# Performance work log

Measured on AMD Instinct MI355X. Metric: run time of the kernel, lower is better.

Reference implementation:

```python
import jax, jax.numpy as jnp
import numpy as np

Ts = 1.0  # simulation time step from netParams['simulation']


def _alpha_filter(x, tau):
    # Causal SRM-alpha PSP filter along time (leading axis):
    #   y[t] = Ts * sum_{k>=0} (k*Ts/tau) * exp(1 - k*Ts/tau) * x[t-k]
    # Implemented as an exact 2-state linear recurrence (IIR form of the alpha kernel).
    d = jnp.float32(np.exp(-Ts / tau))
    c = jnp.float32(np.e * Ts / tau * Ts)  # kernel scale * Ts integration factor

    def step(carry, xt):
        P, Q = carry           # P[t] = sum x[j] d^{t-j}; Q[t] = sum x[j] (t-j) d^{t-j}
        Q = d * (Q + P)
        P = d * P + xt
        return (P, Q), c * Q

    z = jnp.zeros_like(x[0])
    _, y = jax.lax.scan(step, (z, z), x)
    return y


def _make_spike(theta, tauRho, scaleRho):
    # SLAYER spike function: Heaviside forward, surrogate-gradient backward
    pdf_scale = scaleRho / (tauRho * theta)
    pdf_tc = tauRho * theta

    @jax.custom_vjp
    def spike(u):
        return (u >= theta).astype(u.dtype)

    def fwd(u):
        return spike(u), u

    def bwd(u, g):
        return (g * pdf_scale * jnp.exp(-jnp.abs(u - theta) / pdf_tc),)

    spike.defvjp(fwd, bwd)
    return spike


def _lif_spike(u_in, theta, tauRef, scaleRef, tauRho, scaleRho):
    # Sequential leaky integrate-and-fire with alpha refractory kernel:
    #   u[t] = u_in[t] - scaleRef*theta * sum_{j<t} s[j] * (dt/tauRef)*exp(1-dt/tauRef), dt=(t-j)*Ts
    # Refractory alpha kernel realized by the same 2-state recurrence, fed by emitted spikes.
    d = jnp.float32(np.exp(-Ts / tauRef))
    ref_gain = jnp.float32(scaleRef * theta * np.e * Ts / tauRef)
    spike = _make_spike(theta, tauRho, scaleRho)

    def step(carry, ut):
        P, Q = carry
        Q = d * (Q + P)            # refractory kernel value (zero at lag 0)
        s = spike(ut - ref_gain * Q)
        P = d * P + s              # inject this step's spikes
        return (P, Q), s

    z = jnp.zeros_like(u_in[0])
    _, s = jax.lax.scan(step, (z, z), u_in)
    return s


def _conv2d_t(x, w, pad):
    # x: [T, N, C, H, W] -> same spatial conv applied at every timestep (slayer conv = Conv3d with kT=1)
    T, N, C, H, W = x.shape
    y = jax.lax.conv_general_dilated(
        x.reshape(T * N, C, H, W), w,
        window_strides=(1, 1), padding=[(pad, pad), (pad, pad)],
        dimension_numbers=('NCHW', 'OIHW', 'NCHW'))
    return y.reshape(T, N, -1, H, W)


def _forward(spikeInput, conv1_w, conv2_w):
    # spikeInput: [N, C, H, W, T] -> scan over leading time axis
    x = jnp.transpose(spikeInput, (4, 0, 1, 2, 3))
    psp1 = _alpha_filter(x, tau=1.0)                                        # slayer1.psp (tauSr=1)
    s1 = _lif_spike(_conv2d_t(psp1, conv1_w, 2),
                    theta=30.0, tauRef=1.0, scaleRef=1.0, tauRho=1.0, scaleRho=10.0)
    psp2 = _alpha_filter(s1, tau=2.0)                                       # slayer2.psp (tauSr=2)
    s2 = _lif_spike(_conv2d_t(psp2, conv2_w, 1),
                    theta=50.0, tauRef=2.0, scaleRef=1.0, tauRho=1.0, scaleRho=10.0)
    return jnp.transpose(s2, (1, 2, 3, 4, 0))  # back to [N, C, H, W, T]


def setup_inputs() -> dict:
    key = jax.random.key(0)
    k1, k2, k3 = jax.random.split(key, 3)
    spikeInput = (jax.random.uniform(k1, (2, 8, 128, 128, 64)) < 0.1).astype(jnp.float32)
    # slayer conv uses weightScale-amplified weights, bias-free; scale so thresholds are reachable
    conv1_w = jax.random.normal(k2, (8, 8, 5, 5), jnp.float32) * 2.0
    conv2_w = jax.random.normal(k3, (8, 8, 3, 3), jnp.float32) * 2.0
    return {"spikeInput": spikeInput, "conv1_w": conv1_w, "conv2_w": conv2_w}


def reference(spikeInput, conv1_w, conv2_w):
    return _forward(spikeInput, conv1_w, conv2_w)
```

## Files before the change

kernel.cpp:

```cpp
#include <hip/hip_runtime.h>

#define TN 64
#define NB 2
#define CH 8
#define HH 128
#define WW 128
#define HW (HH*WW)
#define CHW (CH*HW)
#define NCHW (NB*CHW)

__global__ __launch_bounds__(256) void k_psp1(const float* __restrict__ x,
                                              float* __restrict__ psp1) {
    int e = blockIdx.x * blockDim.x + threadIdx.x;
    if (e >= NCHW) return;
    const float d1 = 0.36787944117144233f;
    const float c1 = 2.7182818284590452f;
    float P = 0.f, Q = 0.f;
    const float4* xe = reinterpret_cast<const float4*>(x + (size_t)e * TN);
    #pragma unroll
    for (int t4 = 0; t4 < TN / 4; ++t4) {
        float4 xv = xe[t4];
        float xs[4] = {xv.x, xv.y, xv.z, xv.w};
        #pragma unroll
        for (int j = 0; j < 4; ++j) {
            Q = d1 * (Q + P);
            P = d1 * P + xs[j];
            psp1[(size_t)(t4 * 4 + j) * NCHW + e] = c1 * Q;
        }
    }
}

__global__ __launch_bounds__(256, 4) void k_conv1(const float* __restrict__ in,
                                                  const float* __restrict__ w1,
                                                  float* __restrict__ outp) {
    __shared__ __align__(16) float tile[2][12][136];
    const int img = blockIdx.y;
    const int h0 = blockIdx.x * 8;
    const int tid = threadIdx.x;
    const int lx = tid & 31;
    const int yi = tid >> 5;
    const int x0 = lx * 4;
    const float* base = in + (size_t)img * CHW;
    float* lds = &tile[0][0][0];

    float acc[CH][4];
    #pragma unroll
    for (int co = 0; co < CH; ++co)
        #pragma unroll
        for (int xo = 0; xo < 4; ++xo) acc[co][xo] = 0.f;

    for (int cig = 0; cig < 4; ++cig) {
        const int ci0 = cig * 2;
        if (cig) __syncthreads();
        for (int slot = tid; slot < 1632; slot += 256) {
            int r = slot / 136;
            int c = slot - r * 136;
            int gh = h0 + r - 2, gw = c - 2;
            bool ok = (gh >= 0 && gh < HH && gw >= 0 && gw < WW);
            int g = gh * WW + gw;
            lds[slot]        = ok ? base[ci0 * HW + g]       : 0.f;
            lds[1632 + slot] = ok ? base[(ci0 + 1) * HW + g] : 0.f;
        }
        __syncthreads();

        #pragma unroll
        for (int c = 0; c < 2; ++c) {
            const int ci = ci0 + c;
            const float* chp = lds + c * 1632;
            #pragma unroll
            for (int ky = 0; ky < 5; ++ky) {
                const float4* rp =
                    reinterpret_cast<const float4*>(chp + (yi + ky) * 136 + x0);
                float4 a = rp[0], b = rp[1];
                float f[8] = {a.x, a.y, a.z, a.w, b.x, b.y, b.z, b.w};
                #pragma unroll
                for (int co = 0; co < CH; ++co) {
                    const float* wp = w1 + (co * CH + ci) * 25 + ky * 5;
                    #pragma unroll
                    for (int kx = 0; kx < 5; ++kx) {
                        float wv = wp[kx];
                        #pragma unroll
                        for (int xo = 0; xo < 4; ++xo)
                            acc[co][xo] = fmaf(wv, f[kx + xo], acc[co][xo]);
                    }
                }
            }
        }
    }

    float* ob = outp + (size_t)img * CHW + (h0 + yi) * WW + x0;
    #pragma unroll
    for (int co = 0; co < CH; ++co)
        *reinterpret_cast<float4*>(ob + co * HW) =
            make_float4(acc[co][0], acc[co][1], acc[co][2], acc[co][3]);
}

__global__ __launch_bounds__(256) void k_lif1_psp2(const float* __restrict__ u1,
                                                   float* __restrict__ psp2) {
    int e = blockIdx.x * blockDim.x + threadIdx.x;
    if (e >= NCHW) return;
    const float dr = 0.36787944117144233f;
    const float rg = 81.54845485377136f;
    const float th = 30.f;
    const float d2 = 0.60653065971263342f;
    const float c2 = 1.35914091422952262f;
    float Pr = 0.f, Qr = 0.f, P2 = 0.f, Q2 = 0.f;
    #pragma unroll 8
    for (int t = 0; t < TN; ++t) {
        Qr = dr * (Qr + Pr);
        float u = u1[(size_t)t * NCHW + e];
        float s = (u - rg * Qr >= th) ? 1.0f : 0.0f;
        Pr = dr * Pr + s;
        Q2 = d2 * (Q2 + P2);
        P2 = d2 * P2 + s;
        psp2[(size_t)t * NCHW + e] = c2 * Q2;
    }
}

__global__ __launch_bounds__(256, 4) void k_conv2(const float* __restrict__ in,
                                                  const float* __restrict__ w2,
                                                  float* __restrict__ outp) {
    __shared__ __align__(16) float tile[2][10][136];
    const int img = blockIdx.y;
    const int h0 = blockIdx.x * 8;
    const int tid = threadIdx.x;
    const int lx = tid & 31;
    const int yi = tid >> 5;
    const int x0 = lx * 4;
    const float* base = in + (size_t)img * CHW;
    float* lds = &tile[0][0][0];

    float acc[CH][4];
    #pragma unroll
    for (int co = 0; co < CH; ++co)
        #pragma unroll
        for (int xo = 0; xo < 4; ++xo) acc[co][xo] = 0.f;

    for (int cig = 0; cig < 4; ++cig) {
        const int ci0 = cig * 2;
        if (cig) __syncthreads();
        for (int slot = tid; slot < 1360; slot += 256) {
            int r = slot / 136;
            int c = slot - r * 136;
            int gh = h0 + r - 1, gw = c - 1;
            bool ok = (gh >= 0 && gh < HH && gw >= 0 && gw < WW);
            int g = gh * WW + gw;
            lds[slot]        = ok ? base[ci0 * HW + g]       : 0.f;
            lds[1360 + slot] = ok ? base[(ci0 + 1) * HW + g] : 0.f;
        }
        __syncthreads();

        #pragma unroll
        for (int c = 0; c < 2; ++c) {
            const int ci = ci0 + c;
            const float* chp = lds + c * 1360;
            #pragma unroll
            for (int ky = 0; ky < 3; ++ky) {
                const float4* rp =
                    reinterpret_cast<const float4*>(chp + (yi + ky) * 136 + x0);
                float4 a = rp[0], b = rp[1];
                float f[8] = {a.x, a.y, a.z, a.w, b.x, b.y, b.z, b.w};
                #pragma unroll
                for (int co = 0; co < CH; ++co) {
                    const float* wp = w2 + (co * CH + ci) * 9 + ky * 3;
                    #pragma unroll
                    for (int kx = 0; kx < 3; ++kx) {
                        float wv = wp[kx];
                        #pragma unroll
                        for (int xo = 0; xo < 4; ++xo)
                            acc[co][xo] = fmaf(wv, f[kx + xo], acc[co][xo]);
                    }
                }
            }
        }
    }

    float* ob = outp + (size_t)img * CHW + (h0 + yi) * WW + x0;
    #pragma unroll
    for (int co = 0; co < CH; ++co)
        *reinterpret_cast<float4*>(ob + co * HW) =
            make_float4(acc[co][0], acc[co][1], acc[co][2], acc[co][3]);
}

__global__ __launch_bounds__(256) void k_lif2(const float* __restrict__ u2,
                                              float* __restrict__ outp) {
    int e = blockIdx.x * blockDim.x + threadIdx.x;
    if (e >= NCHW) return;
    const float dr = 0.60653065971263342f;
    const float rg = 67.95704571147613f;
    const float th = 50.f;
    float Pr = 0.f, Qr = 0.f;
    float sv[TN];
    #pragma unroll
    for (int t = 0; t < TN; ++t) {
        Qr = dr * (Qr + Pr);
        float u = u2[(size_t)t * NCHW + e];
        float s = (u - rg * Qr >= th) ? 1.0f : 0.0f;
        Pr = dr * Pr + s;
        sv[t] = s;
    }
    float4* o = reinterpret_cast<float4*>(outp + (size_t)e * TN);
    #pragma unroll
    for (int i = 0; i < TN / 4; ++i)
        o[i] = make_float4(sv[4 * i], sv[4 * i + 1], sv[4 * i + 2], sv[4 * i + 3]);
}

extern "C" void kernel_launch(void* const* d_in, const int* in_sizes, int n_in,
                              void* d_out, int out_size, void* d_ws, size_t ws_size,
                              hipStream_t stream) {
    const float* x  = (const float*)d_in[0];
    const float* w1 = (const float*)d_in[1];
    const float* w2 = (const float*)d_in[2];
    float* out = (float*)d_out;

    float* bufA = (float*)d_ws;
    float* bufB = bufA + (size_t)TN * NCHW;

    dim3 blk(256);
    dim3 grd_pt(NCHW / 256);
    dim3 grd_cv(16, TN * NB);

    k_psp1<<<grd_pt, blk, 0, stream>>>(x, bufA);
    k_conv1<<<grd_cv, blk, 0, stream>>>(bufA, w1, bufB);
    k_lif1_psp2<<<grd_pt, blk, 0, stream>>>(bufB, bufA);
    k_conv2<<<grd_cv, blk, 0, stream>>>(bufA, w2, bufB);
    k_lif2<<<grd_pt, blk, 0, stream>>>(bufB, out);
}
```

Baseline: 216.1 us.

## Double-buffer conv input tiles with register prefetch of next channel pair

Both conv kernels now double-buffer the shared-memory tile and prefetch the next channel pair's halo values from global memory into registers before the compute phase. Global offsets are precomputed once per thread instead of recomputed each channel group. This removes one barrier per iteration and is meant to overlap global load latency with the FMA loop. The cost is doubled LDS usage and extra registers (up to 14 floats plus 7 offsets), which may hurt occupancy under launch_bounds(256,4).

After: 204.7 us. -5.3%, faster.

```diff
diff --git a/kernel.cpp b/kernel.cpp
--- a/kernel.cpp
+++ b/kernel.cpp
@@ -33,15 +33,34 @@
 __global__ __launch_bounds__(256, 4) void k_conv1(const float* __restrict__ in,
                                                   const float* __restrict__ w1,
                                                   float* __restrict__ outp) {
-    __shared__ __align__(16) float tile[2][12][136];
+    __shared__ __align__(16) float tile[2][2][12][136];
     const int img = blockIdx.y;
     const int h0 = blockIdx.x * 8;
     const int tid = threadIdx.x;
-    const int lx = tid & 31;
     const int yi = tid >> 5;
-    const int x0 = lx * 4;
+    const int x0 = (tid & 31) * 4;
     const float* base = in + (size_t)img * CHW;
-    float* lds = &tile[0][0][0];
+
+    int goff[7];
+    #pragma unroll
+    for (int k = 0; k < 7; ++k) {
+        int idx = tid + (k << 8);
+        int r = idx / 136;
+        int c = idx - r * 136;
+        int gh = h0 + r - 2, gw = c - 2;
+        bool ok = (idx < 1632) && (gh >= 0) && (gh < HH) && (gw >= 0) && (gw < WW);
+        goff[k] = ok ? (gh * WW + gw) : -1;
+    }
+
+    float va[7], vb[7];
+    #pragma unroll
+    for (int k = 0; k < 7; ++k) {
+        int g = goff[k];
+        int gc = g < 0 ? 0 : g;
+        float t0 = base[gc], t1 = base[HW + gc];
+        va[k] = g < 0 ? 0.f : t0;
+        vb[k] = g < 0 ? 0.f : t1;
+    }
 
     float acc[CH][4];
     #pragma unroll
@@ -50,29 +69,39 @@
         for (int xo = 0; xo < 4; ++xo) acc[co][xo] = 0.f;
 
     for (int cig = 0; cig < 4; ++cig) {
-        const int ci0 = cig * 2;
-        if (cig) __syncthreads();
-        for (int slot = tid; slot < 1632; slot += 256) {
-            int r = slot / 136;
-            int c = slot - r * 136;
-            int gh = h0 + r - 2, gw = c - 2;
-            bool ok = (gh >= 0 && gh < HH && gw >= 0 && gw < WW);
-            int g = gh * WW + gw;
-            lds[slot]        = ok ? base[ci0 * HW + g]       : 0.f;
-            lds[1632 + slot] = ok ? base[(ci0 + 1) * HW + g] : 0.f;
+        float* dst = &tile[cig & 1][0][0][0];
+        #pragma unroll
+        for (int k = 0; k < 7; ++k) {
+            int idx = tid + (k << 8);
+            if (k < 6 || idx < 1632) {
+                dst[idx]        = va[k];
+                dst[1632 + idx] = vb[k];
+            }
+        }
+        if (cig < 3) {
+            const float* nb = base + (size_t)(cig + 1) * 2 * HW;
+            #pragma unroll
+            for (int k = 0; k < 7; ++k) {
+                int g = goff[k];
+                int gc = g < 0 ? 0 : g;
+                float t0 = nb[gc], t1 = nb[HW + gc];
+                va[k] = g < 0 ? 0.f : t0;
+                vb[k] = g < 0 ? 0.f : t1;
+            }
         }
         __syncthreads();
 
+        const float* bufp = &tile[cig & 1][0][0][0];
         #pragma unroll
         for (int c = 0; c < 2; ++c) {
-            const int ci = ci0 + c;
-            const float* chp = lds + c * 1632;
+            const int ci = cig * 2 + c;
+            const float* chp = bufp + c * 1632;
             #pragma unroll
             for (int ky = 0; ky < 5; ++ky) {
                 const float4* rp =
                     reinterpret_cast<const float4*>(chp + (yi + ky) * 136 + x0);
-                float4 a = rp[0], b = rp[1];
-                float f[8] = {a.x, a.y, a.z, a.w, b.x, b.y, b.z, b.w};
+                float4 A = rp[0], B = rp[1];
+                float f[8] = {A.x, A.y, A.z, A.w, B.x, B.y, B.z, B.w};
                 #pragma unroll
                 for (int co = 0; co < CH; ++co) {
                     const float* wp = w1 + (co * CH + ci) * 25 + ky * 5;
@@ -120,15 +149,34 @@
 __global__ __launch_bounds__(256, 4) void k_conv2(const float* __restrict__ in,
                                                   const float* __restrict__ w2,
                                                   float* __restrict__ outp) {
-    __shared__ __align__(16) float tile[2][10][136];
+    __shared__ __align__(16) float tile[2][2][10][136];
     const int img = blockIdx.y;
     const int h0 = blockIdx.x * 8;
     const int tid = threadIdx.x;
-    const int lx = tid & 31;
     const int yi = tid >> 5;
-    const int x0 = lx * 4;
+    const int x0 = (tid & 31) * 4;
     const float* base = in + (size_t)img * CHW;
-    float* lds = &tile[0][0][0];
+
+    int goff[6];
+    #pragma unroll
+    for (int k = 0; k < 6; ++k) {
+        int idx = tid + (k << 8);
+        int r = idx / 136;
+        int c = idx - r * 136;
+        int gh = h0 + r - 1, gw = c - 1;
+        bool ok = (idx < 1360) && (gh >= 0) && (gh < HH) && (gw >= 0) && (gw < WW);
+        goff[k] = ok ? (gh * WW + gw) : -1;
+    }
+
+    float va[6], vb[6];
+    #pragma unroll
+    for (int k = 0; k < 6; ++k) {
+        int g = goff[k];
+        int gc = g < 0 ? 0 : g;
+        float t0 = base[gc], t1 = base[HW + gc];
+        va[k] = g < 0 ? 0.f : t0;
+        vb[k] = g < 0 ? 0.f : t1;
+    }
 
     float acc[CH][4];
     #pragma unroll
@@ -137,29 +185,39 @@
         for (int xo = 0; xo < 4; ++xo) acc[co][xo] = 0.f;
 
     for (int cig = 0; cig < 4; ++cig) {
-        const int ci0 = cig * 2;
-        if (cig) __syncthreads();
-        for (int slot = tid; slot < 1360; slot += 256) {
-            int r = slot / 136;
-            int c = slot - r * 136;
-            int gh = h0 + r - 1, gw = c - 1;
-            bool ok = (gh >= 0 && gh < HH && gw >= 0 && gw < WW);
-            int g = gh * WW + gw;
-            lds[slot]        = ok ? base[ci0 * HW + g]       : 0.f;
-            lds[1360 + slot] = ok ? base[(ci0 + 1) * HW + g] : 0.f;
+        float* dst = &tile[cig & 1][0][0][0];
+        #pragma unroll
+        for (int k = 0; k < 6; ++k) {
+            int idx = tid + (k << 8);
+            if (k < 5 || idx < 1360) {
+                dst[idx]        = va[k];
+                dst[1360 + idx] = vb[k];
+            }
+        }
+        if (cig < 3) {
+            const float* nb = base + (size_t)(cig + 1) * 2 * HW;
+            #pragma unroll
+            for (int k = 0; k < 6; ++k) {
+                int g = goff[k];
+                int gc = g < 0 ? 0 : g;
+                float t0 = nb[gc], t1 = nb[HW + gc];
+                va[k] = g < 0 ? 0.f : t0;
+                vb[k] = g < 0 ? 0.f : t1;
+            }
         }
         __syncthreads();
 
+        const float* bufp = &tile[cig & 1][0][0][0];
         #pragma unroll
         for (int c = 0; c < 2; ++c) {
-            const int ci = ci0 + c;
-            const float* chp = lds + c * 1360;
+            const int ci = cig * 2 + c;
+            const float* chp = bufp + c * 1360;
             #pragma unroll
             for (int ky = 0; ky < 3; ++ky) {
                 const float4* rp =
                     reinterpret_cast<const float4*>(chp + (yi + ky) * 136 + x0);
-                float4 a = rp[0], b = rp[1];
-                float f[8] = {a.x, a.y, a.z, a.w, b.x, b.y, b.z, b.w};
+                float4 A = rp[0], B = rp[1];
+                float f[8] = {A.x, A.y, A.z, A.w, B.x, B.y, B.z, B.w};
                 #pragma unroll
                 for (int co = 0; co < CH; ++co) {
                     const float* wp = w2 + (co * CH + ci) * 9 + ky * 3;
```
